# Kernel tuning notes

Measured on AMD Instinct MI355X. Metric: run time of the kernel, lower is better.

The kernel has to match this reference:

```python
import jax, jax.numpy as jnp
import numpy as np

V, E, HD, NT = 50001, 256, 512, 24   # vocab, embed_dim, hidden_dim, tag_size
H = HD // 2                          # per-direction LSTM hidden
B, S = 64, 512


def setup_inputs() -> dict:
    key = jax.random.key(0)
    ks = jax.random.split(key, 18)
    lw = lambda k, sh, s=0.05: (jax.random.normal(k, sh, jnp.float32) * s)
    x = jax.random.randint(ks[0], (B, S), 0, V).astype(jnp.int32)
    lengths = jax.random.randint(ks[1], (B,), S // 2, S + 1)
    mask = jnp.arange(S)[None, :] < lengths[:, None]  # [B,S] bool, mask[:,0]=True
    return {
        "x": x,
        "mask": mask,
        "emb": lw(ks[2], (V, E), 0.1),
        "Wih_f": lw(ks[3], (4 * H, E)), "Whh_f": lw(ks[4], (4 * H, H)),
        "bih_f": lw(ks[5], (4 * H,)), "bhh_f": lw(ks[6], (4 * H,)),
        "Wih_b": lw(ks[7], (4 * H, E)), "Whh_b": lw(ks[8], (4 * H, H)),
        "bih_b": lw(ks[9], (4 * H,)), "bhh_b": lw(ks[10], (4 * H,)),
        "Wout": lw(ks[11], (NT, HD)), "bout": lw(ks[12], (NT,)),
        "trans": lw(ks[13], (NT, NT), 0.1),
        "start": lw(ks[14], (NT,), 0.1),
        "end": lw(ks[15], (NT,), 0.1),
    }


def _lstm_dir(xs, Wih, Whh, bih, bhh):
    # xs: [S, B, E] -> hs: [S, B, H]; torch gate order i, f, g, o
    Bn = xs.shape[1]
    h0 = jnp.zeros((Bn, H), xs.dtype)

    def step(carry, xt):
        h, c = carry
        g = xt @ Wih.T + h @ Whh.T + bih + bhh
        i, f, gg, o = jnp.split(g, 4, axis=-1)
        c = jax.nn.sigmoid(f) * c + jax.nn.sigmoid(i) * jnp.tanh(gg)
        h = jax.nn.sigmoid(o) * jnp.tanh(c)
        return (h, c), h

    _, hs = jax.lax.scan(step, (h0, h0), xs)
    return hs


def _viterbi(emissions, mask, trans, start, end):
    # emissions: [B, S, T]; mask: [B, S] bool. Returns (tags [B,S] int, best_score [B]).
    em = emissions.transpose(1, 0, 2)   # [S, B, T]
    mk = mask.transpose(1, 0)           # [S, B]
    nT = trans.shape[0]
    idx_id = jnp.arange(nT)[None, :]    # identity backpointers for padded steps
    score = start[None, :] + em[0]      # [B, T]

    def step(score, inp):
        e_t, m_t = inp
        cand = score[:, :, None] + trans[None, :, :] + e_t[:, None, :]  # [B,Tprev,Tnext]
        idx = jnp.argmax(cand, axis=1)
        best = jnp.max(cand, axis=1)
        idx = jnp.where(m_t[:, None], idx, idx_id)
        new_score = jnp.where(m_t[:, None], best, score)
        return new_score, idx

    score, hist = jax.lax.scan(step, score, (em[1:], mk[1:]))  # hist: [S-1, B, T]
    final = score + end[None, :]
    last_tag = jnp.argmax(final, axis=1)   # [B]
    best_score = jnp.max(final, axis=1)    # [B]

    def back(tag, h_t):
        prev = jnp.take_along_axis(h_t, tag[:, None], axis=1)[:, 0]
        return prev, tag

    tag0, ys = jax.lax.scan(back, last_tag, hist, reverse=True)
    tags = jnp.concatenate([tag0[None, :], ys], axis=0).T  # [B, S]
    return tags, best_score


def reference(x, mask, emb, Wih_f, Whh_f, bih_f, bhh_f, Wih_b, Whh_b, bih_b, bhh_b,
              Wout, bout, trans, start, end):
    e = emb[x]                      # [B, S, E] embedding gather
    xs = e.transpose(1, 0, 2)       # [S, B, E] time-major for scan
    hf = _lstm_dir(xs, Wih_f, Whh_f, bih_f, bhh_f)
    hb = jnp.flip(_lstm_dir(jnp.flip(xs, 0), Wih_b, Whh_b, bih_b, bhh_b), 0)
    h = jnp.concatenate([hf, hb], axis=-1)          # [S, B, HD]
    emis = (h @ Wout.T + bout).transpose(1, 0, 2)   # [B, S, T]
    tags, _ = _viterbi(emis, mask, trans, start, end)
    return tags
```

## Files before the change

### kernel.cpp

```cpp
#include <hip/hip_runtime.h>
#include <math.h>

#define B_   64
#define S_   512
#define E_   256
#define H_   256
#define G4H_ 1024
#define NT_  24

static const size_t HBUF_OFF  = 0;
static const size_t CST_OFF   = 131072;
static const size_t EMF_OFF   = 163840;
static const size_t EMB_OFF   = 950272;
static const size_t HOUT_OFF  = 1736704;

__device__ __forceinline__ float sigmoidf_(float x) {
  return 1.0f / (1.0f + expf(-x));
}

__global__ __launch_bounds__(256) void k1_xpre(
    const int* __restrict__ x, const float* __restrict__ emb,
    const float* __restrict__ Wih_f, const float* __restrict__ bih_f,
    const float* __restrict__ bhh_f, const float* __restrict__ Wih_b,
    const float* __restrict__ bih_b, const float* __restrict__ bhh_b,
    float* __restrict__ xpre_c, int chunk, int tc)
{
  __shared__ float As[32][132];
  __shared__ float Bs[32][132];
  __shared__ int   xt[128];

  const int tid = threadIdx.x;
  const int wg  = blockIdx.x;
  const int per_dir = 4 * tc;
  const int d   = wg / per_dir;
  const int rem = wg % per_dir;
  const int m0  = (rem >> 3) * 128;
  const int n0  = (rem & 7) * 128;
  const int t0  = chunk * tc;

  const float* Wih = d ? Wih_b : Wih_f;
  const float* bih = d ? bih_b : bih_f;
  const float* bhh = d ? bhh_b : bhh_f;

  if (tid < 128) {
    int m = m0 + tid;
    int lt = m >> 6, b = m & 63;
    int tok = d ? (S_ - 1 - (t0 + lt)) : (t0 + lt);
    xt[tid] = x[b * S_ + tok];
  }
  __syncthreads();

  float acc[8][8];
#pragma unroll
  for (int i = 0; i < 8; ++i)
#pragma unroll
    for (int j = 0; j < 8; ++j) acc[i][j] = 0.0f;

  const int mt8 = tid & 15;
  const int nt8 = tid >> 4;
  const int q = tid & 7, rbase = tid >> 3;

  for (int kc = 0; kc < 8; ++kc) {
    const int k0 = kc * 32;
#pragma unroll
    for (int i = 0; i < 4; ++i) {
      int row = rbase + i * 32;
      float4 a = *(const float4*)(emb + (long)xt[row] * E_ + k0 + q * 4);
      As[q * 4 + 0][row] = a.x; As[q * 4 + 1][row] = a.y;
      As[q * 4 + 2][row] = a.z; As[q * 4 + 3][row] = a.w;
      float4 w = *(const float4*)(Wih + (long)(n0 + row) * E_ + k0 + q * 4);
      Bs[q * 4 + 0][row] = w.x; Bs[q * 4 + 1][row] = w.y;
      Bs[q * 4 + 2][row] = w.z; Bs[q * 4 + 3][row] = w.w;
    }
    __syncthreads();
#pragma unroll
    for (int k = 0; k < 32; ++k) {
      float4 a0 = *(float4*)&As[k][mt8 * 8];
      float4 a1 = *(float4*)&As[k][mt8 * 8 + 4];
      float4 b0 = *(float4*)&Bs[k][nt8 * 8];
      float4 b1 = *(float4*)&Bs[k][nt8 * 8 + 4];
      float am[8] = {a0.x, a0.y, a0.z, a0.w, a1.x, a1.y, a1.z, a1.w};
      float bn[8] = {b0.x, b0.y, b0.z, b0.w, b1.x, b1.y, b1.z, b1.w};
#pragma unroll
      for (int i = 0; i < 8; ++i)
#pragma unroll
        for (int j = 0; j < 8; ++j) acc[i][j] = fmaf(am[i], bn[j], acc[i][j]);
    }
    __syncthreads();
  }

  float bias[8];
  {
    float4 u0 = *(const float4*)(bih + n0 + nt8 * 8);
    float4 u1 = *(const float4*)(bih + n0 + nt8 * 8 + 4);
    float4 v0 = *(const float4*)(bhh + n0 + nt8 * 8);
    float4 v1 = *(const float4*)(bhh + n0 + nt8 * 8 + 4);
    bias[0] = u0.x + v0.x; bias[1] = u0.y + v0.y; bias[2] = u0.z + v0.z;
    bias[3] = u0.w + v0.w; bias[4] = u1.x + v1.x; bias[5] = u1.y + v1.y;
    bias[6] = u1.z + v1.z; bias[7] = u1.w + v1.w;
  }
#pragma unroll
  for (int i = 0; i < 8; ++i) {
    int m = m0 + mt8 * 8 + i;
    int lt = m >> 6, b = m & 63;
    float* o = xpre_c + ((size_t)(d * tc + lt) * B_ + b) * G4H_ + n0 + nt8 * 8;
    float4 r0, r1;
    r0.x = acc[i][0] + bias[0]; r0.y = acc[i][1] + bias[1];
    r0.z = acc[i][2] + bias[2]; r0.w = acc[i][3] + bias[3];
    r1.x = acc[i][4] + bias[4]; r1.y = acc[i][5] + bias[5];
    r1.z = acc[i][6] + bias[6]; r1.w = acc[i][7] + bias[7];
    *(float4*)o = r0;
    *(float4*)(o + 4) = r1;
  }
}

__global__ __launch_bounds__(256) void k2_lstm(
    const float* __restrict__ Whh_f, const float* __restrict__ Whh_b,
    const float* __restrict__ xpre_c, float* __restrict__ hout_c,
    unsigned long long* hbuf, float* cstate, int chunk, int tc)
{
  __shared__ float Wt[256][32];
  __shared__ float hT[256][20];
  __shared__ float part[512 * 4];

  const int tid = threadIdx.x;
  const int wg  = blockIdx.x;
  const int d   = wg >> 7;
  const int bg  = (wg >> 5) & 3;
  const int s   = wg & 31;
  const int b0  = bg * 16;
  const float* Whh = d ? Whh_b : Whh_f;

  {
    int q = tid & 7, r = tid >> 3;
    int g = r >> 3, j = r & 7;
    long R = (long)(g * H_ + s * 8 + j);
#pragma unroll
    for (int i = 0; i < 8; ++i) {
      int k = q * 4 + i * 32;
      float4 w = *(const float4*)(Whh + R * E_ + k);
      Wt[k + 0][r] = w.x; Wt[k + 1][r] = w.y;
      Wt[k + 2][r] = w.z; Wt[k + 3][r] = w.w;
    }
  }
  const int w    = tid >> 6;
  const int lane = tid & 63;
  const int bl16 = lane & 15;
  const int kb   = lane >> 4;
  const int ks   = tid >> 5, tl = tid & 31, bt = tl & 3, rt = tl >> 2;
  const int pbl  = tid >> 3, pj = tid & 7;

  float c_reg = 0.0f;
  if (chunk > 0 && tid < 128)
    c_reg = cstate[((size_t)d * B_ + b0 + pbl) * H_ + s * 8 + pj];
  __syncthreads();

  for (int tt = 1; tt <= tc; ++tt) {
    const int t  = chunk * tc + tt;
    const int lt = tt - 1;

    float xp[4];
    if (tid < 128) {
#pragma unroll
      for (int g = 0; g < 4; ++g)
        xp[g] = xpre_c[((size_t)(d * tc + lt) * B_ + b0 + pbl) * G4H_ +
                       g * H_ + s * 8 + pj];
    }

    {
      const unsigned expt = (unsigned)(t - 1);
      const unsigned long long* hb =
          hbuf + ((size_t)(((t - 1) & 1) * 2 + d)) * (256 * 64);
      const int kbase = w * 64 + kb * 16;
      const size_t a0 = (size_t)kbase * 64 + b0 + bl16;
      unsigned long long e[16];
#pragma unroll
      for (int i = 0; i < 16; ++i)
        e[i] = __hip_atomic_load(hb + a0 + (size_t)i * 64,
                                 __ATOMIC_RELAXED, __HIP_MEMORY_SCOPE_AGENT);
      int lim = 0;
      while (true) {
        unsigned bad = 0;
#pragma unroll
        for (int i = 0; i < 16; ++i)
          if ((unsigned)(e[i] >> 32) != expt) bad |= (1u << i);
        if (bad == 0) break;
        if (++lim > (1 << 18)) break;
#pragma unroll
        for (int i = 0; i < 16; ++i)
          if (bad & (1u << i))
            e[i] = __hip_atomic_load(hb + a0 + (size_t)i * 64,
                                     __ATOMIC_RELAXED,
                                     __HIP_MEMORY_SCOPE_AGENT);
      }
#pragma unroll
      for (int i = 0; i < 16; ++i)
        hT[kbase + i][bl16] = __uint_as_float((unsigned)e[i]);
    }

    float4 accr[4];
#pragma unroll
    for (int bi = 0; bi < 4; ++bi) accr[bi] = make_float4(0.f, 0.f, 0.f, 0.f);
    {
      const int kb2 = ks * 32;
#pragma unroll 8
      for (int kk = 0; kk < 32; ++kk) {
        int k = kb2 + kk;
        float4 h4 = *(float4*)&hT[k][bt * 4];
        float4 w4 = *(float4*)&Wt[k][rt * 4];
        float ha[4] = {h4.x, h4.y, h4.z, h4.w};
#pragma unroll
        for (int bi = 0; bi < 4; ++bi) {
          accr[bi].x = fmaf(ha[bi], w4.x, accr[bi].x);
          accr[bi].y = fmaf(ha[bi], w4.y, accr[bi].y);
          accr[bi].z = fmaf(ha[bi], w4.z, accr[bi].z);
          accr[bi].w = fmaf(ha[bi], w4.w, accr[bi].w);
        }
      }
    }
#pragma unroll
    for (int bi = 0; bi < 4; ++bi) {
      accr[bi].x += __shfl_xor(accr[bi].x, 32, 64);
      accr[bi].y += __shfl_xor(accr[bi].y, 32, 64);
      accr[bi].z += __shfl_xor(accr[bi].z, 32, 64);
      accr[bi].w += __shfl_xor(accr[bi].w, 32, 64);
    }
    if (lane < 32) {
#pragma unroll
      for (int bi = 0; bi < 4; ++bi) {
        int eb = (bt * 4 + bi) * 32 + rt * 4;
        part[(eb + 0) * 4 + w] = accr[bi].x;
        part[(eb + 1) * 4 + w] = accr[bi].y;
        part[(eb + 2) * 4 + w] = accr[bi].z;
        part[(eb + 3) * 4 + w] = accr[bi].w;
      }
    }
    __syncthreads();

    if (tid < 128) {
      int bglob = b0 + pbl;
      float gsum[4];
#pragma unroll
      for (int g = 0; g < 4; ++g) {
        float4 p = *(float4*)&part[(pbl * 32 + g * 8 + pj) * 4];
        gsum[g] = xp[g] + ((p.x + p.y) + (p.z + p.w));
      }
      float si = sigmoidf_(gsum[0]);
      float sf = sigmoidf_(gsum[1]);
      float tg = tanhf(gsum[2]);
      float so = sigmoidf_(gsum[3]);
      c_reg = sf * c_reg + si * tg;
      float h = so * tanhf(c_reg);
      hout_c[((size_t)(d * tc + lt) * B_ + bglob) * H_ + s * 8 + pj] = h;
      unsigned long long pk =
          (((unsigned long long)(unsigned)t) << 32) |
          (unsigned long long)__float_as_uint(h);
      __hip_atomic_store(hbuf + ((size_t)((t & 1) * 2 + d)) * (256 * 64) +
                             (size_t)(s * 8 + pj) * 64 + bglob,
                         pk, __ATOMIC_RELAXED, __HIP_MEMORY_SCOPE_AGENT);
    }
    __syncthreads();
  }

  if (tid < 128)
    cstate[((size_t)d * B_ + b0 + pbl) * H_ + s * 8 + pj] = c_reg;
}

__global__ __launch_bounds__(256) void k3_emis(
    const float* __restrict__ hout_c, const float* __restrict__ Wout,
    float* __restrict__ emisX, int d, int chunk, int tc)
{
  __shared__ float hh[8][264];
  const int tid = threadIdx.x;
  const int nt8 = tc >> 3;
  const int b  = blockIdx.x / nt8;
  const int t8 = blockIdx.x % nt8;
  const int lt0 = t8 * 8;
  {
    int r = tid >> 5, q = tid & 31;
    const float* src = hout_c + ((size_t)(d * tc + lt0 + r) * B_ + b) * H_;
#pragma unroll
    for (int i = 0; i < 2; ++i) {
      int f4i = q + 32 * i;
      *(float4*)&hh[r][f4i * 4] = *(const float4*)(src + f4i * 4);
    }
  }
  __syncthreads();
  if (tid < 192) {
    int r = tid / 24, tag = tid % 24;
    float acc = 0.0f;
    const float* w = Wout + (size_t)tag * 512 + d * 256;
#pragma unroll 4
    for (int k4 = 0; k4 < 64; ++k4) {
      float4 wv = *(const float4*)(w + k4 * 4);
      float4 hv = *(const float4*)&hh[r][k4 * 4];
      acc = fmaf(wv.x, hv.x, acc);
      acc = fmaf(wv.y, hv.y, acc);
      acc = fmaf(wv.z, hv.z, acc);
      acc = fmaf(wv.w, hv.w, acc);
    }
    int lt = lt0 + r;
    int tok = d ? (S_ - 1 - (chunk * tc + lt)) : (chunk * tc + lt);
    emisX[((size_t)b * S_ + tok) * NT_ + tag] = acc;
  }
}

__global__ __launch_bounds__(64) void k4_viterbi(
    const float* __restrict__ emisF, const float* __restrict__ emisB,
    const float* __restrict__ bout, const unsigned char* __restrict__ mb,
    const float* __restrict__ trans, const float* __restrict__ startv,
    const float* __restrict__ endv, int* __restrict__ outp)
{
  __shared__ float tl[24 * 25];
  __shared__ float sc[24];
  __shared__ float fin[24];
  __shared__ unsigned char hist[511 * 24];
  const int b = blockIdx.x;
  const int tid = threadIdx.x;
  const int is_bool = mb[1];

  for (int i = tid; i < 576; i += 64) tl[(i / 24) * 25 + (i % 24)] = trans[i];
  if (tid < 24) {
    size_t e0 = (size_t)b * S_ * NT_ + tid;
    sc[tid] = startv[tid] + (emisF[e0] + emisB[e0] + bout[tid]);
  }
  __syncthreads();

  for (int t = 1; t < S_; ++t) {
    float best = -3.4e38f, scj = 0.f;
    int idx = 0;
    int m;
    {
      int mi = b * S_ + t;
      m = is_bool ? (int)mb[mi] : (int)mb[mi << 2];
    }
    if (tid < 24) {
      size_t ei = ((size_t)b * S_ + t) * NT_ + tid;
      float e = emisF[ei] + emisB[ei] + bout[tid];
      for (int i = 0; i < 24; ++i) {
        float v = (sc[i] + tl[i * 25 + tid]) + e;
        if (v > best) { best = v; idx = i; }
      }
      scj = sc[tid];
    }
    __syncthreads();
    if (tid < 24) {
      sc[tid] = m ? best : scj;
      hist[(t - 1) * 24 + tid] = (unsigned char)(m ? idx : tid);
    }
    __syncthreads();
  }
  if (tid < 24) fin[tid] = sc[tid] + endv[tid];
  __syncthreads();
  if (tid == 0) {
    int tag = 0; float best = fin[0];
    for (int i = 1; i < 24; ++i)
      if (fin[i] > best) { best = fin[i]; tag = i; }
    outp[b * S_ + (S_ - 1)] = tag;
    for (int tt = S_ - 2; tt >= 0; --tt) {
      tag = hist[tt * 24 + tag];
      outp[b * S_ + tt] = tag;
    }
  }
}

extern "C" void kernel_launch(void* const* d_in, const int* in_sizes, int n_in,
                              void* d_out, int out_size, void* d_ws,
                              size_t ws_size, hipStream_t stream)
{
  const int*   x      = (const int*)d_in[0];
  const unsigned char* maskb = (const unsigned char*)d_in[1];
  const float* emb    = (const float*)d_in[2];
  const float* Wih_f  = (const float*)d_in[3];
  const float* Whh_f  = (const float*)d_in[4];
  const float* bih_f  = (const float*)d_in[5];
  const float* bhh_f  = (const float*)d_in[6];
  const float* Wih_b  = (const float*)d_in[7];
  const float* Whh_b  = (const float*)d_in[8];
  const float* bih_b  = (const float*)d_in[9];
  const float* bhh_b  = (const float*)d_in[10];
  const float* Wout   = (const float*)d_in[11];
  const float* bout   = (const float*)d_in[12];
  const float* trans  = (const float*)d_in[13];
  const float* startv = (const float*)d_in[14];
  const float* endv   = (const float*)d_in[15];

  int tc = 8;
  {
    const int cand[6] = {512, 256, 128, 64, 32, 16};
    for (int i = 0; i < 6; ++i) {
      size_t needF = HOUT_OFF + (size_t)cand[i] * (2 * B_ * H_ + 2 * B_ * G4H_);
      if (needF * sizeof(float) <= ws_size) { tc = cand[i]; break; }
    }
  }
  const int nc = S_ / tc;

  float* ws     = (float*)d_ws;
  unsigned long long* hbuf = (unsigned long long*)(ws + HBUF_OFF);
  float* cstate = ws + CST_OFF;
  float* emisF  = ws + EMF_OFF;
  float* emisB  = ws + EMB_OFF;
  float* hout_c = ws + HOUT_OFF;
  float* xpre_c = hout_c + (size_t)tc * 2 * B_ * H_;

  hipMemsetAsync(d_ws, 0, 131072 * sizeof(float), stream);

  for (int c = 0; c < nc; ++c) {
    hipLaunchKernelGGL(k1_xpre, dim3(8 * tc), dim3(256), 0, stream,
                       x, emb, Wih_f, bih_f, bhh_f, Wih_b, bih_b, bhh_b,
                       xpre_c, c, tc);
    hipLaunchKernelGGL(k2_lstm, dim3(256), dim3(256), 0, stream,
                       Whh_f, Whh_b, xpre_c, hout_c, hbuf, cstate, c, tc);
    hipLaunchKernelGGL(k3_emis, dim3(64 * (tc / 8)), dim3(256), 0, stream,
                       hout_c, Wout, emisF, 0, c, tc);
    hipLaunchKernelGGL(k3_emis, dim3(64 * (tc / 8)), dim3(256), 0, stream,
                       hout_c, Wout, emisB, 1, c, tc);
  }
  hipLaunchKernelGGL(k4_viterbi, dim3(64), dim3(64), 0, stream,
                     emisF, emisB, bout, maskb, trans, startv, endv,
                     (int*)d_out);
}
```

Before: 3.137 ms.

## Keep LSTM recurrent weights in registers and double-buffer partial sums

```diff
diff --git a/kernel.cpp b/kernel.cpp
--- a/kernel.cpp
+++ b/kernel.cpp
@@ -114,14 +114,13 @@
   }
 }
 
-__global__ __launch_bounds__(256) void k2_lstm(
+__global__ __launch_bounds__(256, 1) void k2_lstm(
     const float* __restrict__ Whh_f, const float* __restrict__ Whh_b,
     const float* __restrict__ xpre_c, float* __restrict__ hout_c,
     unsigned long long* hbuf, float* cstate, int chunk, int tc)
 {
-  __shared__ float Wt[256][32];
-  __shared__ float hT[256][20];
-  __shared__ float part[512 * 4];
+  __shared__ float hTb[16][260];
+  __shared__ float part[2][4][16][36];
 
   const int tid = threadIdx.x;
   const int wg  = blockIdx.x;
@@ -131,33 +130,36 @@
   const int b0  = bg * 16;
   const float* Whh = d ? Whh_b : Whh_f;
 
-  {
-    int q = tid & 7, r = tid >> 3;
-    int g = r >> 3, j = r & 7;
-    long R = (long)(g * H_ + s * 8 + j);
-#pragma unroll
-    for (int i = 0; i < 8; ++i) {
-      int k = q * 4 + i * 32;
-      float4 w = *(const float4*)(Whh + R * E_ + k);
-      Wt[k + 0][r] = w.x; Wt[k + 1][r] = w.y;
-      Wt[k + 2][r] = w.z; Wt[k + 3][r] = w.w;
-    }
-  }
-  const int w    = tid >> 6;
-  const int lane = tid & 63;
-  const int bl16 = lane & 15;
-  const int kb   = lane >> 4;
-  const int ks   = tid >> 5, tl = tid & 31, bt = tl & 3, rt = tl >> 2;
-  const int pbl  = tid >> 3, pj = tid & 7;
+  const int w     = tid >> 6;
+  const int lane  = tid & 63;
+  const int bl16  = lane & 15;
+  const int kb    = lane >> 4;
+  const int kbase = w * 64 + kb * 16;
+  const int ks    = tid >> 5;
+  const int tl    = tid & 31, bt = tl & 3, rt = tl >> 2;
+  const int pbl   = tid >> 3, pj = tid & 7;
+
+  float wreg[4][32];
+#pragma unroll
+  for (int ri = 0; ri < 4; ++ri) {
+    int r = rt * 4 + ri, g = r >> 3, j = r & 7;
+    const float* src = Whh + ((size_t)(g * H_ + s * 8 + j)) * H_ + ks * 32;
+#pragma unroll
+    for (int q = 0; q < 8; ++q) {
+      float4 v = *(const float4*)(src + q * 4);
+      wreg[ri][q * 4 + 0] = v.x; wreg[ri][q * 4 + 1] = v.y;
+      wreg[ri][q * 4 + 2] = v.z; wreg[ri][q * 4 + 3] = v.w;
+    }
+  }
 
   float c_reg = 0.0f;
   if (chunk > 0 && tid < 128)
     c_reg = cstate[((size_t)d * B_ + b0 + pbl) * H_ + s * 8 + pj];
-  __syncthreads();
 
   for (int tt = 1; tt <= tc; ++tt) {
     const int t  = chunk * tc + tt;
     const int lt = tt - 1;
+    const int p  = tt & 1;
 
     float xp[4];
     if (tid < 128) {
@@ -171,7 +173,6 @@
       const unsigned expt = (unsigned)(t - 1);
       const unsigned long long* hb =
           hbuf + ((size_t)(((t - 1) & 1) * 2 + d)) * (256 * 64);
-      const int kbase = w * 64 + kb * 16;
       const size_t a0 = (size_t)kbase * 64 + b0 + bl16;
       unsigned long long e[16];
 #pragma unroll
@@ -193,57 +194,67 @@
                                      __ATOMIC_RELAXED,
                                      __HIP_MEMORY_SCOPE_AGENT);
       }
-#pragma unroll
-      for (int i = 0; i < 16; ++i)
-        hT[kbase + i][bl16] = __uint_as_float((unsigned)e[i]);
-    }
-
-    float4 accr[4];
-#pragma unroll
-    for (int bi = 0; bi < 4; ++bi) accr[bi] = make_float4(0.f, 0.f, 0.f, 0.f);
-    {
-      const int kb2 = ks * 32;
-#pragma unroll 8
-      for (int kk = 0; kk < 32; ++kk) {
-        int k = kb2 + kk;
-        float4 h4 = *(float4*)&hT[k][bt * 4];
-        float4 w4 = *(float4*)&Wt[k][rt * 4];
-        float ha[4] = {h4.x, h4.y, h4.z, h4.w};
+      float4 v0, v1, v2, v3;
+      v0.x = __uint_as_float((unsigned)e[0]);  v0.y = __uint_as_float((unsigned)e[1]);
+      v0.z = __uint_as_float((unsigned)e[2]);  v0.w = __uint_as_float((unsigned)e[3]);
+      v1.x = __uint_as_float((unsigned)e[4]);  v1.y = __uint_as_float((unsigned)e[5]);
+      v1.z = __uint_as_float((unsigned)e[6]);  v1.w = __uint_as_float((unsigned)e[7]);
+      v2.x = __uint_as_float((unsigned)e[8]);  v2.y = __uint_as_float((unsigned)e[9]);
+      v2.z = __uint_as_float((unsigned)e[10]); v2.w = __uint_as_float((unsigned)e[11]);
+      v3.x = __uint_as_float((unsigned)e[12]); v3.y = __uint_as_float((unsigned)e[13]);
+      v3.z = __uint_as_float((unsigned)e[14]); v3.w = __uint_as_float((unsigned)e[15]);
+      *(float4*)&hTb[bl16][kbase +  0] = v0;
+      *(float4*)&hTb[bl16][kbase +  4] = v1;
+      *(float4*)&hTb[bl16][kbase +  8] = v2;
+      *(float4*)&hTb[bl16][kbase + 12] = v3;
+    }
+
+    float acc[4][4];
+#pragma unroll
+    for (int bi = 0; bi < 4; ++bi)
+#pragma unroll
+      for (int ri = 0; ri < 4; ++ri) acc[bi][ri] = 0.0f;
+#pragma unroll
+    for (int kq = 0; kq < 8; ++kq) {
+      const int k0 = ks * 32 + kq * 4;
+      float4 h4[4];
+#pragma unroll
+      for (int bi = 0; bi < 4; ++bi)
+        h4[bi] = *(float4*)&hTb[bt * 4 + bi][k0];
+#pragma unroll
+      for (int kk = 0; kk < 4; ++kk) {
 #pragma unroll
         for (int bi = 0; bi < 4; ++bi) {
-          accr[bi].x = fmaf(ha[bi], w4.x, accr[bi].x);
-          accr[bi].y = fmaf(ha[bi], w4.y, accr[bi].y);
-          accr[bi].z = fmaf(ha[bi], w4.z, accr[bi].z);
-          accr[bi].w = fmaf(ha[bi], w4.w, accr[bi].w);
+          const float hv = kk == 0 ? h4[bi].x : kk == 1 ? h4[bi].y
+                         : kk == 2 ? h4[bi].z : h4[bi].w;
+#pragma unroll
+          for (int ri = 0; ri < 4; ++ri)
+            acc[bi][ri] = fmaf(hv, wreg[ri][kq * 4 + kk], acc[bi][ri]);
         }
       }
     }
 #pragma unroll
-    for (int bi = 0; bi < 4; ++bi) {
-      accr[bi].x += __shfl_xor(accr[bi].x, 32, 64);
-      accr[bi].y += __shfl_xor(accr[bi].y, 32, 64);
-      accr[bi].z += __shfl_xor(accr[bi].z, 32, 64);
-      accr[bi].w += __shfl_xor(accr[bi].w, 32, 64);
-    }
+    for (int bi = 0; bi < 4; ++bi)
+#pragma unroll
+      for (int ri = 0; ri < 4; ++ri)
+        acc[bi][ri] += __shfl_xor(acc[bi][ri], 32, 64);
     if (lane < 32) {
 #pragma unroll
       for (int bi = 0; bi < 4; ++bi) {
-        int eb = (bt * 4 + bi) * 32 + rt * 4;
-        part[(eb + 0) * 4 + w] = accr[bi].x;
-        part[(eb + 1) * 4 + w] = accr[bi].y;
-        part[(eb + 2) * 4 + w] = accr[bi].z;
-        part[(eb + 3) * 4 + w] = accr[bi].w;
+        float4 v = make_float4(acc[bi][0], acc[bi][1], acc[bi][2], acc[bi][3]);
+        *(float4*)&part[p][w][bt * 4 + bi][rt * 4] = v;
       }
     }
     __syncthreads();
 
     if (tid < 128) {
-      int bglob = b0 + pbl;
+      const int bglob = b0 + pbl;
       float gsum[4];
 #pragma unroll
       for (int g = 0; g < 4; ++g) {
-        float4 p = *(float4*)&part[(pbl * 32 + g * 8 + pj) * 4];
-        gsum[g] = xp[g] + ((p.x + p.y) + (p.z + p.w));
+        const int r = g * 8 + pj;
+        gsum[g] = xp[g] + ((part[p][0][pbl][r] + part[p][1][pbl][r]) +
+                           (part[p][2][pbl][r] + part[p][3][pbl][r]));
       }
       float si = sigmoidf_(gsum[0]);
       float sf = sigmoidf_(gsum[1]);
@@ -251,15 +262,14 @@
       float so = sigmoidf_(gsum[3]);
       c_reg = sf * c_reg + si * tg;
       float h = so * tanhf(c_reg);
-      hout_c[((size_t)(d * tc + lt) * B_ + bglob) * H_ + s * 8 + pj] = h;
       unsigned long long pk =
           (((unsigned long long)(unsigned)t) << 32) |
           (unsigned long long)__float_as_uint(h);
       __hip_atomic_store(hbuf + ((size_t)((t & 1) * 2 + d)) * (256 * 64) +
                              (size_t)(s * 8 + pj) * 64 + bglob,
                          pk, __ATOMIC_RELAXED, __HIP_MEMORY_SCOPE_AGENT);
-    }
-    __syncthreads();
+      hout_c[((size_t)(d * tc + lt) * B_ + bglob) * H_ + s * 8 + pj] = h;
+    }
   }
 
   if (tid < 128)
@@ -268,14 +278,17 @@
 
 __global__ __launch_bounds__(256) void k3_emis(
     const float* __restrict__ hout_c, const float* __restrict__ Wout,
-    float* __restrict__ emisX, int d, int chunk, int tc)
+    float* __restrict__ emisF, float* __restrict__ emisB, int chunk, int tc)
 {
   __shared__ float hh[8][264];
   const int tid = threadIdx.x;
   const int nt8 = tc >> 3;
-  const int b  = blockIdx.x / nt8;
-  const int t8 = blockIdx.x % nt8;
-  const int lt0 = t8 * 8;
+  const int per_d = 64 * nt8;
+  const int d   = blockIdx.x / per_d;
+  const int rem = blockIdx.x % per_d;
+  const int b   = rem / nt8;
+  const int lt0 = (rem % nt8) * 8;
+  float* emisX = d ? emisB : emisF;
   {
     int r = tid >> 5, q = tid & 31;
     const float* src = hout_c + ((size_t)(d * tc + lt0 + r) * B_ + b) * H_;
@@ -411,10 +424,8 @@
                        xpre_c, c, tc);
     hipLaunchKernelGGL(k2_lstm, dim3(256), dim3(256), 0, stream,
                        Whh_f, Whh_b, xpre_c, hout_c, hbuf, cstate, c, tc);
-    hipLaunchKernelGGL(k3_emis, dim3(64 * (tc / 8)), dim3(256), 0, stream,
-                       hout_c, Wout, emisF, 0, c, tc);
-    hipLaunchKernelGGL(k3_emis, dim3(64 * (tc / 8)), dim3(256), 0, stream,
-                       hout_c, Wout, emisB, 1, c, tc);
+    hipLaunchKernelGGL(k3_emis, dim3(2 * 64 * (tc / 8)), dim3(256), 0, stream,
+                       hout_c, Wout, emisF, emisB, c, tc);
   }
   hipLaunchKernelGGL(k4_viterbi, dim3(64), dim3(64), 0, stream,
                      emisF, emisB, bout, maskb, trans, startv, endv,
```

Result: faster. 2.885 ms (-8.0%).
